# Performance work log

Hardware: AMD Instinct MI355X
Metric: run time of the kernel (lower is better)

## Reference

```python
import jax, jax.numpy as jnp
import numpy as np

DIM = 256
NUM_ATOMS = 1024
SPARSITY = 8
BETA = 0.25
EPS = 1e-10


def setup_inputs() -> dict:
    key = jax.random.key(0)
    k1, k2, k3, k4 = jax.random.split(key, 4)
    z_e = jax.random.normal(k1, (32, DIM, 32, 32), dtype=jnp.float32)
    dict_w = jax.random.normal(k2, (NUM_ATOMS, DIM), dtype=jnp.float32)
    rep_w = jax.random.normal(k3, (NUM_ATOMS, DIM), dtype=jnp.float32) * (1.0 / np.sqrt(DIM))
    rep_b = jnp.zeros((NUM_ATOMS,), dtype=jnp.float32)
    return {"z_e": z_e, "dict_w": dict_w, "rep_w": rep_w, "rep_b": rep_b}


def reference(z_e, dict_w, rep_w, rep_b):
    # NCHW -> NHWC, flatten to [N, D]
    ze = jnp.transpose(z_e, (0, 2, 3, 1))
    ze_shape = ze.shape
    flat = ze.reshape(-1, DIM)  # [N, D]
    n = flat.shape[0]

    # representation: Linear + softmax over atoms
    rep = jax.nn.softmax(flat @ rep_w.T + rep_b, axis=1)  # [N, K]

    # squared distances to dictionary atoms
    dists = (jnp.sum(flat ** 2, axis=1, keepdims=True)
             + jnp.sum(dict_w ** 2, axis=1)
             - 2.0 * (flat @ dict_w.T))  # [N, K]

    # top-L smallest distances
    _, idx = jax.lax.top_k(-dists, SPARSITY)  # [N, L]

    # one-hot scatter of selected atoms
    encodings = jnp.zeros((n, NUM_ATOMS), dtype=flat.dtype)
    encodings = encodings.at[jnp.arange(n)[:, None], idx].set(1.0)

    rep_sparse = encodings * rep / SPARSITY  # [N, K]
    z_dl = (rep_sparse @ dict_w).reshape(ze_shape)  # [B, H, W, D]

    e_latent_loss = jnp.mean((jax.lax.stop_gradient(z_dl) - ze) ** 2)
    loss = BETA * e_latent_loss

    # straight-through estimator
    z_st = ze + jax.lax.stop_gradient(z_dl - ze)

    avg_probs = jnp.mean(encodings, axis=0)
    avg_probs = avg_probs / jnp.sum(avg_probs)
    perplexity = jnp.exp(-jnp.sum(avg_probs * jnp.log(avg_probs + EPS)))

    return loss, jnp.transpose(z_st, (0, 3, 1, 2)), perplexity, rep_sparse
```

## Files before the change

kernel.cpp:

```cpp
#include <hip/hip_runtime.h>
#include <hip/hip_bf16.h>
#include <stdint.h>

#define NROWS   32768
#define DIMD    256
#define NATOMS  1024

typedef short  bf16x8 __attribute__((ext_vector_type(8)));
typedef float  f32x4  __attribute__((ext_vector_type(4)));

__device__ __forceinline__ unsigned short bf16rne(float f) {
    unsigned u = __float_as_uint(f);
    u = u + 0x7FFFu + ((u >> 16) & 1u);
    return (unsigned short)(u >> 16);
}

__global__ __launch_bounds__(256) void vq_bprep(
    const float* __restrict__ rep_w, const float* __restrict__ dict_w,
    unsigned short* __restrict__ Bs, float* __restrict__ dnorm,
    int* __restrict__ counts)
{
    const int tid = threadIdx.x;
    if (blockIdx.x == 0) {
        for (int i = tid; i < NATOMS; i += 256) counts[i] = 0;
    }
    const int atom = blockIdx.x * 32 + (tid >> 3);
    const int kc = tid & 7;
    float ss = 0.f;
#pragma unroll
    for (int m = 0; m < 2; ++m) {
        const float* src = (m ? dict_w : rep_w) + (size_t)atom * DIMD + kc * 32;
        unsigned short* dst = Bs + (size_t)m * 262144 + (size_t)kc * 32768 + atom * 32;
#pragma unroll
        for (int q = 0; q < 8; ++q) {
            float4 v = *(const float4*)&src[q * 4];
            float fv[4] = {v.x, v.y, v.z, v.w};
            unsigned short a0[4];
#pragma unroll
            for (int e = 0; e < 4; ++e) {
                if (m) ss = fmaf(fv[e], fv[e], ss);
                a0[e] = bf16rne(fv[e]);
            }
            *(ushort4*)&dst[q * 4] = make_ushort4(a0[0], a0[1], a0[2], a0[3]);
        }
    }
    ss += __shfl_down(ss, 4, 8);
    ss += __shfl_down(ss, 2, 8);
    ss += __shfl_down(ss, 1, 8);
    if (kc == 0) dnorm[atom] = ss;
}

__device__ __forceinline__ void insk(unsigned u, unsigned (&kd)[8]) {
#pragma unroll
    for (int j = 7; j >= 1; --j)
        kd[j] = min(max(u, kd[j - 1]), kd[j]);
    kd[0] = min(u, kd[0]);
}

__device__ __forceinline__ void wave_merge_k(int lane, unsigned (&kd)[8], float& se) {
#pragma unroll
    for (int half = 32; half >= 16; half >>= 1) {
        const int src = (lane + half) & 63;
        unsigned ko[8];
#pragma unroll
        for (int j = 0; j < 8; ++j) ko[j] = (unsigned)__shfl((int)kd[j], src, 64);
        const float so = __shfl(se, src, 64);
        if (lane < half) {
            se += so;
#pragma unroll
            for (int t = 0; t < 8; ++t) insk(ko[t], kd);
        }
    }
}

__global__ __launch_bounds__(256, 2) void vq_main(
    const float* __restrict__ z_e, const unsigned short* __restrict__ Bs,
    const float* __restrict__ rep_b, const float* __restrict__ dnorm,
    int* __restrict__ idx_out, float* __restrict__ fsum_out)
{
    __shared__ __align__(16) float rbS[1024];
    __shared__ __align__(16) float dnS[1024];
    __shared__ unsigned mKu[3][64][8];
    __shared__ float mS[3][64];
    __shared__ unsigned fK[64][8];
    __shared__ float fSum[64];

    const int tid = threadIdx.x;
    const int lane = tid & 63, w = tid >> 6;
    const int c = lane & 15, lg = lane >> 4;
    const int row0 = blockIdx.x * 64;
    const int bb = row0 >> 10, hw0 = row0 & 1023;

    for (int i = tid; i < 1024; i += 256) { rbS[i] = rep_b[i]; dnS[i] = dnorm[i]; }

    const char* pL = (const char*)Bs;
    const char* pD = (const char*)Bs + 524288;
    const int abase = w << 8;

    bf16x8 bL[8], bD[8];
    {
        const int off = ((abase + c) << 6) + (lg << 4);
#pragma unroll
        for (int kc = 0; kc < 8; ++kc) {
            bL[kc] = *(const bf16x8*)(pL + ((size_t)kc << 16) + off);
            bD[kc] = *(const bf16x8*)(pD + ((size_t)kc << 16) + off);
        }
    }

    bf16x8 A[4][8];
    {
        const float* zb = z_e + (size_t)bb * 262144 + hw0 + c;
#pragma unroll
        for (int kc = 0; kc < 8; ++kc) {
            float f[4][8];
#pragma unroll
            for (int e = 0; e < 8; ++e) {
                const float* p = zb + (size_t)(kc * 32 + lg * 8 + e) * 1024;
                f[0][e] = p[0];
                f[1][e] = p[16];
                f[2][e] = p[32];
                f[3][e] = p[48];
            }
#pragma unroll
            for (int rf = 0; rf < 4; ++rf)
#pragma unroll
                for (int e = 0; e < 8; ++e)
                    A[rf][kc][e] = (short)bf16rne(f[rf][e]);
        }
    }
    __syncthreads();

    unsigned kd[4][8];
    float se[4] = {0.f, 0.f, 0.f, 0.f};
#pragma unroll
    for (int rf = 0; rf < 4; ++rf)
#pragma unroll
        for (int j = 0; j < 8; ++j) kd[rf][j] = 0xFFFFFFFFu;

    for (int it = 0; it < 16; ++it) {
        const int tb = abase + (it << 4) + (lg << 2);
        const f32x4 rbv = *(const f32x4*)&rbS[tb];
        const f32x4 dnv = *(const f32x4*)&dnS[tb];

#pragma unroll
        for (int rf = 0; rf < 4; ++rf) {
            f32x4 aL = {0.f, 0.f, 0.f, 0.f};
            f32x4 aD = {0.f, 0.f, 0.f, 0.f};
#pragma unroll
            for (int kc = 0; kc < 8; ++kc) {
                aL = __builtin_amdgcn_mfma_f32_16x16x32_bf16(bL[kc], A[rf][kc], aL, 0, 0, 0);
                aD = __builtin_amdgcn_mfma_f32_16x16x32_bf16(bD[kc], A[rf][kc], aD, 0, 0, 0);
            }
#pragma unroll
            for (int q = 0; q < 4; ++q) {
                const unsigned atom = (unsigned)(tb + q);
                se[rf] += __expf(aL[q] + rbv[q]);
                unsigned u = __float_as_uint(dnv[q] - 2.0f * aD[q]);
                u ^= ((unsigned)((int)u >> 31) | 0x80000000u);
                insk((u & ~1023u) | atom, kd[rf]);
            }
        }

        if (it < 15) {
            const int off = ((abase + (it + 1) * 16 + c) << 6) + (lg << 4);
#pragma unroll
            for (int kc = 0; kc < 8; ++kc) {
                bL[kc] = *(const bf16x8*)(pL + ((size_t)kc << 16) + off);
                bD[kc] = *(const bf16x8*)(pD + ((size_t)kc << 16) + off);
            }
        }
    }

#pragma unroll
    for (int rf = 0; rf < 4; ++rf)
        wave_merge_k(lane, kd[rf], se[rf]);

    if (w >= 1 && lane < 16) {
#pragma unroll
        for (int rf = 0; rf < 4; ++rf) {
#pragma unroll
            for (int j = 0; j < 8; ++j)
                mKu[w - 1][rf * 16 + c][j] = kd[rf][j];
            mS[w - 1][rf * 16 + c] = se[rf];
        }
    }
    __syncthreads();

    if (w == 0 && lane < 16) {
#pragma unroll
        for (int rf = 0; rf < 4; ++rf) {
            const int rloc = rf * 16 + c;
            for (int p = 0; p < 3; ++p)
#pragma unroll
                for (int t = 0; t < 8; ++t)
                    insk(mKu[p][rloc][t], kd[rf]);
            se[rf] += mS[0][rloc] + mS[1][rloc] + mS[2][rloc];
#pragma unroll
            for (int j = 0; j < 8; ++j) fK[rloc][j] = kd[rf][j];
            fSum[rloc] = se[rf];
        }
    }
    __syncthreads();

    {
        const int j = tid >> 5, rr = tid & 31;
        idx_out[(row0 + rr) * 8 + j]      = (int)(fK[rr][j] & 1023u);
        idx_out[(row0 + 32 + rr) * 8 + j] = (int)(fK[32 + rr][j] & 1023u);
    }
    if (tid < 64) fsum_out[row0 + tid] = fSum[tid];
}

__global__ __launch_bounds__(256, 4) void vq_recon(
    const float* __restrict__ z_e, const float* __restrict__ dict_w,
    const float* __restrict__ rep_w, const float* __restrict__ rep_b,
    const int* __restrict__ idx_in, const float* __restrict__ fsum_in,
    float* __restrict__ rep_sparse, float* __restrict__ z_st,
    float* __restrict__ partials, int* __restrict__ counts)
{
    __shared__ __align__(16) float zL[32][260];
    __shared__ int   iS[256];
    __shared__ float wS[256];
    __shared__ float fS[32];
    __shared__ float red[256];

    const int tid = threadIdx.x;
    const int row0 = blockIdx.x * 32;
    const int bb = row0 >> 10, hw0 = row0 & 1023;
    const float* zb = z_e + (size_t)bb * 262144 + hw0;

    {
        float4 z4 = {0.f, 0.f, 0.f, 0.f};
        float4* rp4 = (float4*)rep_sparse + (size_t)row0 * (NATOMS / 4) + tid;
        for (int r = 0; r < 32; ++r)
            rp4[(size_t)r * (NATOMS / 4)] = z4;
    }

    iS[tid] = idx_in[row0 * 8 + tid];
    if (tid < 32) fS[tid] = fsum_in[row0 + tid];
    {
        const int m = tid & 31, dg = tid >> 5;
        for (int it = 0; it < 32; ++it) {
            const int d = it * 8 + dg;
            zL[m][d] = zb[(size_t)d * 1024 + m];
        }
    }
    __syncthreads();

    {
        const int j = tid >> 5, rr = tid & 31;
        const int idx = iS[rr * 8 + j];
        const float* rw = rep_w + (size_t)idx * DIMD;
        float acc = 0.f;
        for (int k = 0; k < DIMD; k += 4) {
            const float4 rv = *(const float4*)&rw[k];
            const f32x4 zv = *(const f32x4*)&zL[rr][k];
            acc = fmaf(zv[0], rv.x, acc);
            acc = fmaf(zv[1], rv.y, acc);
            acc = fmaf(zv[2], rv.z, acc);
            acc = fmaf(zv[3], rv.w, acc);
        }
        wS[rr * 8 + j] = __expf(acc + rep_b[idx]) * 0.125f / fS[rr];
    }
    __syncthreads();

    {
        const int j = tid >> 5, rr = tid & 31;
        rep_sparse[(size_t)(row0 + rr) * NATOMS + iS[rr * 8 + j]] = wS[rr * 8 + j];
    }

    float sacc = 0.f;
    for (int r = 0; r < 32; ++r) {
        float acc = 0.f;
#pragma unroll
        for (int j = 0; j < 8; ++j) {
            const int ix = iS[r * 8 + j];
            const float wv = wS[r * 8 + j];
            acc = fmaf(wv, dict_w[(size_t)ix * DIMD + tid], acc);
        }
        const float ze = zL[r][tid];
        const float diff = acc - ze;
        sacc = fmaf(diff, diff, sacc);
        zL[r][tid] = acc;
    }
    __syncthreads();

    {
        float* ob = z_st + (size_t)bb * 262144 + hw0;
        const int m = tid & 31, dg = tid >> 5;
        for (int it = 0; it < 32; ++it) {
            const int d = it * 8 + dg;
            ob[(size_t)d * 1024 + m] = zL[m][d];
        }
    }

    red[tid] = sacc;
    __syncthreads();
    for (int s = 128; s > 0; s >>= 1) {
        if (tid < s) red[tid] += red[tid + s];
        __syncthreads();
    }
    if (tid == 0) partials[blockIdx.x] = red[0];

    __syncthreads();
    int* hS = (int*)zL;
    for (int i = tid; i < 1024; i += 256) hS[i] = 0;
    __syncthreads();
    atomicAdd(&hS[iS[tid]], 1);
    __syncthreads();
    for (int i = tid; i < 1024; i += 256)
        if (hS[i]) atomicAdd(&counts[i], hS[i]);
}

__global__ void vq_final(const float* __restrict__ partials,
                         const int* __restrict__ counts,
                         float* __restrict__ out_loss, float* __restrict__ out_perp)
{
    __shared__ double dred[256];
    __shared__ float fred[256];
    const int tid = threadIdx.x;
    double s = 0.0;
    for (int i = tid; i < 1024; i += 256) s += (double)partials[i];
    dred[tid] = s;
    __syncthreads();
    for (int st = 128; st > 0; st >>= 1) {
        if (tid < st) dred[tid] += dred[tid + st];
        __syncthreads();
    }
    float ps = 0.f;
    for (int i = tid; i < NATOMS; i += 256) {
        const float p = (float)counts[i] * (1.0f / 262144.0f);
        ps += p * logf(p + 1e-10f);
    }
    fred[tid] = ps;
    __syncthreads();
    for (int st = 128; st > 0; st >>= 1) {
        if (tid < st) fred[tid] += fred[tid + st];
        __syncthreads();
    }
    if (tid == 0) {
        *out_loss = 0.25f * (float)(dred[0] / 8388608.0);
        *out_perp = expf(-fred[0]);
    }
}

extern "C" void kernel_launch(void* const* d_in, const int* in_sizes, int n_in,
                              void* d_out, int out_size, void* d_ws, size_t ws_size,
                              hipStream_t stream) {
    const float* z_e    = (const float*)d_in[0];
    const float* dict_w = (const float*)d_in[1];
    const float* rep_w  = (const float*)d_in[2];
    const float* rep_b  = (const float*)d_in[3];

    float* out = (float*)d_out;
    float* out_loss   = out;
    float* z_st       = out + 1;
    float* out_perp   = out + 1 + 8388608;
    float* rep_sparse = out + 2 + 8388608;

    unsigned short* Bs = (unsigned short*)((((uintptr_t)(z_st + 4194304)) + 255) & ~(uintptr_t)255);

    char* ws = (char*)d_ws;
    int*   idx_out  = (int*)ws;
    float* fsum_out = (float*)(ws + (1 << 20));
    int*   counts   = (int*)(ws + (1 << 20) + (1 << 17));
    float* dnorm    = (float*)(ws + (1 << 20) + (1 << 17) + 4096);
    float* partials = (float*)(ws + (1 << 20) + (1 << 17) + 8192);

    vq_bprep<<<32, 256, 0, stream>>>(rep_w, dict_w, Bs, dnorm, counts);
    vq_main<<<NROWS / 64, 256, 0, stream>>>(z_e, Bs, rep_b, dnorm,
                                            idx_out, fsum_out);
    vq_recon<<<NROWS / 32, 256, 0, stream>>>(z_e, dict_w, rep_w, rep_b,
                                             idx_out, fsum_out,
                                             rep_sparse, z_st, partials, counts);
    vq_final<<<1, 256, 0, stream>>>(partials, counts, out_loss, out_perp);
}
```

Before: 150.7 us.

## Fuse reconstruction stage into main top-k kernel to drop index round-trip

Merges the reconstruction kernel into the main distance/top-k kernel, so each 64-row block handles its own rows in two 32-row halves, reading indices and softmax sums directly from shared memory. This removes a kernel launch and the global write and read of the index and sum buffers, and moves the Bs scratch buffer from the output region into the workspace. The cost is higher shared-memory use per block (an extra ~33KB), which may cut occupancy of the main kernel, and a serial recon tail after the top-k phase with no overlap across blocks at kernel boundaries.

```diff
diff --git a/kernel.cpp b/kernel.cpp
--- a/kernel.cpp
+++ b/kernel.cpp
@@ -76,7 +76,9 @@
 __global__ __launch_bounds__(256, 2) void vq_main(
     const float* __restrict__ z_e, const unsigned short* __restrict__ Bs,
     const float* __restrict__ rep_b, const float* __restrict__ dnorm,
-    int* __restrict__ idx_out, float* __restrict__ fsum_out)
+    const float* __restrict__ rep_w, const float* __restrict__ dict_w,
+    float* __restrict__ rep_sparse, float* __restrict__ z_st,
+    float* __restrict__ partials, int* __restrict__ counts)
 {
     __shared__ __align__(16) float rbS[1024];
     __shared__ __align__(16) float dnS[1024];
@@ -84,6 +86,10 @@
     __shared__ float mS[3][64];
     __shared__ unsigned fK[64][8];
     __shared__ float fSum[64];
+    __shared__ __align__(16) float zL[32][260];
+    __shared__ int   iW[256];
+    __shared__ float wS[256];
+    __shared__ float red[256];
 
     const int tid = threadIdx.x;
     const int lane = tid & 63, w = tid >> 6;
@@ -202,98 +208,73 @@
     }
     __syncthreads();
 
-    {
-        const int j = tid >> 5, rr = tid & 31;
-        idx_out[(row0 + rr) * 8 + j]      = (int)(fK[rr][j] & 1023u);
-        idx_out[(row0 + 32 + rr) * 8 + j] = (int)(fK[32 + rr][j] & 1023u);
-    }
-    if (tid < 64) fsum_out[row0 + tid] = fSum[tid];
-}
-
-__global__ __launch_bounds__(256, 4) void vq_recon(
-    const float* __restrict__ z_e, const float* __restrict__ dict_w,
-    const float* __restrict__ rep_w, const float* __restrict__ rep_b,
-    const int* __restrict__ idx_in, const float* __restrict__ fsum_in,
-    float* __restrict__ rep_sparse, float* __restrict__ z_st,
-    float* __restrict__ partials, int* __restrict__ counts)
-{
-    __shared__ __align__(16) float zL[32][260];
-    __shared__ int   iS[256];
-    __shared__ float wS[256];
-    __shared__ float fS[32];
-    __shared__ float red[256];
-
-    const int tid = threadIdx.x;
-    const int row0 = blockIdx.x * 32;
-    const int bb = row0 >> 10, hw0 = row0 & 1023;
-    const float* zb = z_e + (size_t)bb * 262144 + hw0;
-
-    {
-        float4 z4 = {0.f, 0.f, 0.f, 0.f};
-        float4* rp4 = (float4*)rep_sparse + (size_t)row0 * (NATOMS / 4) + tid;
-        for (int r = 0; r < 32; ++r)
-            rp4[(size_t)r * (NATOMS / 4)] = z4;
-    }
-
-    iS[tid] = idx_in[row0 * 8 + tid];
-    if (tid < 32) fS[tid] = fsum_in[row0 + tid];
-    {
-        const int m = tid & 31, dg = tid >> 5;
-        for (int it = 0; it < 32; ++it) {
-            const int d = it * 8 + dg;
-            zL[m][d] = zb[(size_t)d * 1024 + m];
-        }
-    }
-    __syncthreads();
-
-    {
-        const int j = tid >> 5, rr = tid & 31;
-        const int idx = iS[rr * 8 + j];
-        const float* rw = rep_w + (size_t)idx * DIMD;
-        float acc = 0.f;
-        for (int k = 0; k < DIMD; k += 4) {
-            const float4 rv = *(const float4*)&rw[k];
-            const f32x4 zv = *(const f32x4*)&zL[rr][k];
-            acc = fmaf(zv[0], rv.x, acc);
-            acc = fmaf(zv[1], rv.y, acc);
-            acc = fmaf(zv[2], rv.z, acc);
-            acc = fmaf(zv[3], rv.w, acc);
-        }
-        wS[rr * 8 + j] = __expf(acc + rep_b[idx]) * 0.125f / fS[rr];
-    }
-    __syncthreads();
-
-    {
-        const int j = tid >> 5, rr = tid & 31;
-        rep_sparse[(size_t)(row0 + rr) * NATOMS + iS[rr * 8 + j]] = wS[rr * 8 + j];
-    }
-
-    float sacc = 0.f;
-    for (int r = 0; r < 32; ++r) {
-        float acc = 0.f;
-#pragma unroll
-        for (int j = 0; j < 8; ++j) {
-            const int ix = iS[r * 8 + j];
-            const float wv = wS[r * 8 + j];
-            acc = fmaf(wv, dict_w[(size_t)ix * DIMD + tid], acc);
-        }
-        const float ze = zL[r][tid];
-        const float diff = acc - ze;
-        sacc = fmaf(diff, diff, sacc);
-        zL[r][tid] = acc;
-    }
-    __syncthreads();
-
-    {
-        float* ob = z_st + (size_t)bb * 262144 + hw0;
-        const int m = tid & 31, dg = tid >> 5;
-        for (int it = 0; it < 32; ++it) {
-            const int d = it * 8 + dg;
-            ob[(size_t)d * 1024 + m] = zL[m][d];
-        }
-    }
-
-    red[tid] = sacc;
+    const int m31 = tid & 31, dg = tid >> 5;
+    const int j8 = tid >> 5, rr = tid & 31;
+    float lossacc = 0.f;
+
+    for (int h = 0; h < 2; ++h) {
+        const int r0 = h * 32;
+
+        {
+            float4 z4 = {0.f, 0.f, 0.f, 0.f};
+            float4* rp4 = (float4*)rep_sparse
+                        + (size_t)(row0 + r0) * (NATOMS / 4) + tid;
+            for (int r = 0; r < 32; ++r)
+                rp4[(size_t)r * (NATOMS / 4)] = z4;
+        }
+
+        {
+            const float* zb2 = z_e + (size_t)bb * 262144 + hw0 + r0 + m31;
+            for (int it = 0; it < 32; ++it) {
+                const int d = it * 8 + dg;
+                zL[m31][d] = zb2[(size_t)d * 1024];
+            }
+        }
+        __syncthreads();
+
+        {
+            const int idx = (int)(fK[r0 + rr][j8] & 1023u);
+            const float* rw = rep_w + (size_t)idx * DIMD;
+            float acc = 0.f;
+            for (int k = 0; k < DIMD; k += 4) {
+                const float4 rv = *(const float4*)&rw[k];
+                const f32x4 zv = *(const f32x4*)&zL[rr][k];
+                acc = fmaf(zv[0], rv.x, acc);
+                acc = fmaf(zv[1], rv.y, acc);
+                acc = fmaf(zv[2], rv.z, acc);
+                acc = fmaf(zv[3], rv.w, acc);
+            }
+            iW[rr * 8 + j8] = idx;
+            wS[rr * 8 + j8] = __expf(acc + rbS[idx]) * 0.125f / fSum[r0 + rr];
+        }
+        __syncthreads();
+
+        rep_sparse[(size_t)(row0 + r0 + rr) * NATOMS + iW[rr * 8 + j8]]
+            = wS[rr * 8 + j8];
+
+        for (int r = 0; r < 32; ++r) {
+            float acc = 0.f;
+#pragma unroll
+            for (int j = 0; j < 8; ++j)
+                acc = fmaf(wS[r * 8 + j],
+                           dict_w[(size_t)iW[r * 8 + j] * DIMD + tid], acc);
+            const float diff = acc - zL[r][tid];
+            lossacc = fmaf(diff, diff, lossacc);
+            zL[r][tid] = acc;
+        }
+        __syncthreads();
+
+        {
+            float* ob = z_st + (size_t)bb * 262144 + hw0 + r0 + m31;
+            for (int it = 0; it < 32; ++it) {
+                const int d = it * 8 + dg;
+                ob[(size_t)d * 1024] = zL[m31][d];
+            }
+        }
+        __syncthreads();
+    }
+
+    red[tid] = lossacc;
     __syncthreads();
     for (int s = 128; s > 0; s >>= 1) {
         if (tid < s) red[tid] += red[tid + s];
@@ -305,7 +286,8 @@
     int* hS = (int*)zL;
     for (int i = tid; i < 1024; i += 256) hS[i] = 0;
     __syncthreads();
-    atomicAdd(&hS[iS[tid]], 1);
+    atomicAdd(&hS[(int)(fK[tid >> 3][tid & 7] & 1023u)], 1);
+    atomicAdd(&hS[(int)(fK[32 + (tid >> 3)][tid & 7] & 1023u)], 1);
     __syncthreads();
     for (int i = tid; i < 1024; i += 256)
         if (hS[i]) atomicAdd(&counts[i], hS[i]);
@@ -319,7 +301,7 @@
     __shared__ float fred[256];
     const int tid = threadIdx.x;
     double s = 0.0;
-    for (int i = tid; i < 1024; i += 256) s += (double)partials[i];
+    for (int i = tid; i < 512; i += 256) s += (double)partials[i];
     dred[tid] = s;
     __syncthreads();
     for (int st = 128; st > 0; st >>= 1) {
@@ -357,20 +339,15 @@
     float* out_perp   = out + 1 + 8388608;
     float* rep_sparse = out + 2 + 8388608;
 
-    unsigned short* Bs = (unsigned short*)((((uintptr_t)(z_st + 4194304)) + 255) & ~(uintptr_t)255);
-
     char* ws = (char*)d_ws;
-    int*   idx_out  = (int*)ws;
-    float* fsum_out = (float*)(ws + (1 << 20));
-    int*   counts   = (int*)(ws + (1 << 20) + (1 << 17));
-    float* dnorm    = (float*)(ws + (1 << 20) + (1 << 17) + 4096);
-    float* partials = (float*)(ws + (1 << 20) + (1 << 17) + 8192);
+    unsigned short* Bs = (unsigned short*)(ws + (1 << 20));
+    int*   counts   = (int*)(ws);
+    float* dnorm    = (float*)(ws + 4096);
+    float* partials = (float*)(ws + 8192);
 
     vq_bprep<<<32, 256, 0, stream>>>(rep_w, dict_w, Bs, dnorm, counts);
     vq_main<<<NROWS / 64, 256, 0, stream>>>(z_e, Bs, rep_b, dnorm,
-                                            idx_out, fsum_out);
-    vq_recon<<<NROWS / 32, 256, 0, stream>>>(z_e, dict_w, rep_w, rep_b,
-                                             idx_out, fsum_out,
-                                             rep_sparse, z_st, partials, counts);
+                                            rep_w, dict_w,
+                                            rep_sparse, z_st, partials, counts);
     vq_final<<<1, 256, 0, stream>>>(partials, counts, out_loss, out_perp);
 }
```

After: 142.6 us (median of 3 runs). -5.3%, faster.
